# Optimization experiments

Hardware: AMD Instinct MI355X
Metric: run time of the kernel (lower is better)

## Reference

```python
import jax, jax.numpy as jnp
import numpy as np


def setup_inputs() -> dict:
    key = jax.random.key(0)
    ks = jax.random.split(key, 8)
    B, H, W, C = 4, 64, 64, 64
    Cf = C // 8
    x = jax.random.normal(ks[0], (B, H, W, C), dtype=jnp.float32)
    # 1x1 conv kernels stored as [C_in, C_out] (kernel_size=1)
    w_f = jax.random.normal(ks[1], (C, Cf), dtype=jnp.float32) * 0.05
    b_f = jax.random.normal(ks[2], (Cf,), dtype=jnp.float32) * 0.05
    w_g = jax.random.normal(ks[3], (C, Cf), dtype=jnp.float32) * 0.05
    b_g = jax.random.normal(ks[4], (Cf,), dtype=jnp.float32) * 0.05
    w_h = jax.random.normal(ks[5], (C, C), dtype=jnp.float32) * 0.05
    b_h = jax.random.normal(ks[6], (C,), dtype=jnp.float32) * 0.05
    gamma = jax.random.normal(ks[7], (1,), dtype=jnp.float32) * 0.1
    return {"x": x, "w_f": w_f, "b_f": b_f, "w_g": w_g, "b_g": b_g,
            "w_h": w_h, "b_h": b_h, "gamma": gamma}


def reference(x, w_f, b_f, w_g, b_g, w_h, b_h, gamma):
    B, H, W, C = x.shape
    N = H * W
    xf = x.reshape(B, N, C)  # 1x1 conv == per-pixel linear
    f = xf @ w_f + b_f       # [B, N, C/8]
    g = xf @ w_g + b_g       # [B, N, C/8]
    h = xf @ w_h + b_h       # [B, N, C]
    # attention_map[b, i, j] = <g_i, f_j>, softmax over last axis
    scores = jnp.einsum('bic,bjc->bij', g, f)  # [B, N, N]
    attn = jax.nn.softmax(scores, axis=-1)
    out = jnp.einsum('bij,bjc->bic', attn, h)  # [B, N, C]
    out = out.reshape(B, H, W, C)
    return gamma * out + x
```

## Files before the change

kernel.cpp:

```cpp
#include <hip/hip_runtime.h>
#include <hip/hip_bf16.h>

typedef __bf16 bf16;
typedef __bf16 bf16x8 __attribute__((ext_vector_type(8)));
typedef __bf16 bf16x4 __attribute__((ext_vector_type(4)));
typedef float floatx4 __attribute__((ext_vector_type(4)));

typedef int    aint    __attribute__((may_alias));
typedef long   along   __attribute__((may_alias));

#define NPIX 4096
#define BATCH 4
#define LOG2E 1.4426950408889634f
#define HT_BATCH 262144

__device__ inline bf16x8 zero8() {
    bf16x8 v;
    #pragma unroll
    for (int i = 0; i < 8; ++i) v[i] = (bf16)0.0f;
    return v;
}

__global__ __launch_bounds__(256) void proj_kernel(
    const float* __restrict__ x,
    const float* __restrict__ w_f, const float* __restrict__ b_f,
    const float* __restrict__ w_g, const float* __restrict__ b_g,
    const float* __restrict__ w_h, const float* __restrict__ b_h,
    bf16* __restrict__ fq, bf16* __restrict__ gq, unsigned char* __restrict__ hT)
{
    __shared__ bf16 xs[64 * 72];
    __shared__ bf16 wt[80 * 72];
    __shared__ float bs[80];
    const int tid = threadIdx.x;
    const int p0 = blockIdx.x * 64;

    {
        const float4* xg = (const float4*)(x + (long)p0 * 64);
        #pragma unroll
        for (int it = 0; it < 4; ++it) {
            int i4 = tid + it * 256;
            float4 v = xg[i4];
            int row = i4 >> 4, c4 = (i4 & 15) * 4;
            bf16x4 pk;
            pk[0] = (bf16)v.x; pk[1] = (bf16)v.y; pk[2] = (bf16)v.z; pk[3] = (bf16)v.w;
            *(bf16x4*)(&xs[row * 72 + c4]) = pk;
        }
    }
    for (int idx = tid; idx < 80 * 64; idx += 256) {
        int n = idx >> 6, c = idx & 63;
        float v = (n < 8) ? w_f[c * 8 + n]
                : (n < 16) ? w_g[c * 8 + (n - 8)]
                : w_h[c * 64 + (n - 16)];
        wt[n * 72 + c] = (bf16)v;
    }
    if (tid < 80)
        bs[tid] = (tid < 8) ? b_f[tid] : (tid < 16) ? b_g[tid - 8] : b_h[tid - 16];
    __syncthreads();

    const int wv = tid >> 6, lane = tid & 63;
    const int quad = lane >> 4, l15 = lane & 15;
    const int b = blockIdx.x >> 6;
    const int n0pix = (p0 & (NPIX - 1)) + wv * 16 + quad * 4;

    bf16x8 a0 = *(const bf16x8*)(&xs[(wv * 16 + l15) * 72 + quad * 8]);
    bf16x8 a1 = *(const bf16x8*)(&xs[(wv * 16 + l15) * 72 + 32 + quad * 8]);

    #pragma unroll
    for (int nt = 0; nt < 5; ++nt) {
        float bias = bs[nt * 16 + l15];
        floatx4 acc = {bias, bias, bias, bias};
        bf16x8 b0 = *(const bf16x8*)(&wt[(nt * 16 + l15) * 72 + quad * 8]);
        bf16x8 b1 = *(const bf16x8*)(&wt[(nt * 16 + l15) * 72 + 32 + quad * 8]);
        acc = __builtin_amdgcn_mfma_f32_16x16x32_bf16(a0, b0, acc, 0, 0, 0);
        acc = __builtin_amdgcn_mfma_f32_16x16x32_bf16(a1, b1, acc, 0, 0, 0);
        if (nt == 0) {
            #pragma unroll
            for (int r = 0; r < 4; ++r) {
                long P = (long)p0 + wv * 16 + quad * 4 + r;
                if (l15 < 8) fq[P * 8 + l15] = (bf16)acc[r];
                else         gq[P * 8 + (l15 - 8)] = (bf16)(acc[r] * LOG2E);
            }
        } else {
            int c = nt * 16 + l15 - 16;
            int pk = __builtin_amdgcn_cvt_pk_fp8_f32(acc[0], acc[1], 0, false);
            pk     = __builtin_amdgcn_cvt_pk_fp8_f32(acc[2], acc[3], pk, true);
            *(aint*)(hT + (long)b * HT_BATCH + (n0pix >> 5) * 2048
                     + c * 32 + (n0pix & 31)) = pk;
        }
    }
}

__global__ __launch_bounds__(256) void attn_kernel(
    const bf16* __restrict__ fq, const bf16* __restrict__ gq,
    const unsigned char* __restrict__ hT, float* __restrict__ partial)
{
    __shared__ char smem[4 * 2176];
    const int tid  = threadIdx.x;
    const int wv   = tid >> 6, lane = tid & 63;
    const int quad = lane >> 4, l15 = lane & 15;
    const int js   = blockIdx.x >> 8;
    const int ib   = blockIdx.x & 255;
    const int b    = ib >> 6, it = ib & 63;
    const long rowbase = (long)b * NPIX + it * 64 + wv * 16;
    const int jbase = js * 1024;

    bf16x8 gfrag = zero8();
    if (lane < 16) gfrag = *(const bf16x8*)(gq + (rowbase + lane) * 8);

    const bf16* Fb = fq + ((long)b * NPIX + jbase) * 8;
    const unsigned char* Hb = hT + (long)b * HT_BATCH + (jbase >> 5) * 2048
                            + (l15 * 32 + quad * 8);

    floatx4 acc[5];
    #pragma unroll
    for (int nt = 0; nt < 5; ++nt) acc[nt] = (floatx4){0.f, 0.f, 0.f, 0.f};
    const along ones = 0x3838383838383838L;
    char* Pw = smem + wv * 2176;

    for (int t = 0; t < 8; ++t) {
        along bfr[16];
        #pragma unroll
        for (int ks = 0; ks < 4; ++ks)
            #pragma unroll
            for (int nt = 0; nt < 4; ++nt)
                bfr[ks * 4 + nt] = *(const along*)(Hb + (t * 4 + ks) * 2048 + nt * 512);
        #pragma unroll
        for (int j8 = 0; j8 < 8; ++j8) {
            bf16x8 afrag = zero8();
            if (lane < 16) afrag = *(const bf16x8*)(Fb + (t * 128 + j8 * 16 + l15) * 8);
            floatx4 s = __builtin_amdgcn_mfma_f32_16x16x32_bf16(
                afrag, gfrag, (floatx4){0.f, 0.f, 0.f, 0.f}, 0, 0, 0);
            float e0 = __builtin_amdgcn_exp2f(s[0]);
            float e1 = __builtin_amdgcn_exp2f(s[1]);
            float e2 = __builtin_amdgcn_exp2f(s[2]);
            float e3 = __builtin_amdgcn_exp2f(s[3]);
            int pk = __builtin_amdgcn_cvt_pk_fp8_f32(e0, e1, 0, false);
            pk     = __builtin_amdgcn_cvt_pk_fp8_f32(e2, e3, pk, true);
            *(aint*)(Pw + l15 * 136 + j8 * 16 + quad * 4) = pk;
        }
        asm volatile("" ::: "memory");
        #pragma unroll
        for (int ks = 0; ks < 4; ++ks) {
            along pfrag = *(const along*)(Pw + l15 * 136 + ks * 32 + quad * 8);
            #pragma unroll
            for (int nt = 0; nt < 4; ++nt)
                acc[nt] = __builtin_amdgcn_mfma_f32_16x16x32_fp8_fp8(
                    pfrag, bfr[ks * 4 + nt], acc[nt], 0, 0, 0);
            acc[4] = __builtin_amdgcn_mfma_f32_16x16x32_fp8_fp8(pfrag, ones, acc[4], 0, 0, 0);
        }
    }

    float* pb = partial + ((long)js * (BATCH * NPIX) + rowbase) * 68;
    #pragma unroll
    for (int nt = 0; nt < 4; ++nt)
        #pragma unroll
        for (int r = 0; r < 4; ++r)
            pb[(quad * 4 + r) * 68 + nt * 16 + l15] = acc[nt][r];
    if (l15 == 0) {
        #pragma unroll
        for (int r = 0; r < 4; ++r)
            pb[(quad * 4 + r) * 68 + 64] = acc[4][r];
    }
}

__global__ __launch_bounds__(256) void reduce_kernel(
    const float* __restrict__ partial, const float* __restrict__ x,
    const float* __restrict__ gamma_p, float* __restrict__ out)
{
    const int tid = threadIdx.x;
    const long i  = (long)blockIdx.x * 32 + (tid >> 3);
    const int c0  = (tid & 7) * 8;
    const float* p = partial + i * 68;
    float4 n0 = {0.f, 0.f, 0.f, 0.f}, n1 = {0.f, 0.f, 0.f, 0.f};
    float den = 0.f;
    #pragma unroll
    for (int js = 0; js < 4; ++js) {
        const float* pj = p + (long)js * (BATCH * NPIX) * 68;
        float4 a = *(const float4*)(pj + c0);
        float4 c = *(const float4*)(pj + c0 + 4);
        n0.x += a.x; n0.y += a.y; n0.z += a.z; n0.w += a.w;
        n1.x += c.x; n1.y += c.y; n1.z += c.z; n1.w += c.w;
        den += pj[64];
    }
    const float rd = gamma_p[0] / den;
    const float* xr = x + i * 64 + c0;
    float* orow = out + i * 64 + c0;
    float4 xa = *(const float4*)xr, xb = *(const float4*)(xr + 4);
    float4 oa, ob;
    oa.x = n0.x * rd + xa.x; oa.y = n0.y * rd + xa.y;
    oa.z = n0.z * rd + xa.z; oa.w = n0.w * rd + xa.w;
    ob.x = n1.x * rd + xb.x; ob.y = n1.y * rd + xb.y;
    ob.z = n1.z * rd + xb.z; ob.w = n1.w * rd + xb.w;
    *(float4*)orow = oa; *(float4*)(orow + 4) = ob;
}

extern "C" void kernel_launch(void* const* d_in, const int* in_sizes, int n_in,
                              void* d_out, int out_size, void* d_ws, size_t ws_size,
                              hipStream_t stream) {
    const float* x     = (const float*)d_in[0];
    const float* w_f   = (const float*)d_in[1];
    const float* b_f   = (const float*)d_in[2];
    const float* w_g   = (const float*)d_in[3];
    const float* b_g   = (const float*)d_in[4];
    const float* w_h   = (const float*)d_in[5];
    const float* b_h   = (const float*)d_in[6];
    const float* gamma = (const float*)d_in[7];
    float* out = (float*)d_out;

    bf16* fq = (bf16*)d_ws;
    bf16* gq = fq + 16384 * 8;
    unsigned char* hT = (unsigned char*)(gq + 16384 * 8);
    float* partial = (float*)(hT + (long)BATCH * HT_BATCH);

    proj_kernel<<<256, 256, 0, stream>>>(x, w_f, b_f, w_g, b_g, w_h, b_h, fq, gq, hT);
    attn_kernel<<<1024, 256, 0, stream>>>(fq, gq, hT, partial);
    reduce_kernel<<<512, 256, 0, stream>>>(partial, x, gamma, out);
}
```

Measured before the change: 118.1 us.

## Double-buffer P tiles and H fragments to overlap score and PV phases

Splits the attention inner loop into load, score/exp and PV phases, and software-pipelines them with two LDS P buffers and two register sets of H fragments. The next tile's scores and H loads are issued before the current tile's PV MFMAs, which is meant to hide global-load and exp latency behind matrix work. It also adds a launch_bounds occupancy hint of 4 and doubles per-wave shared memory. The extra 16 longs of fragment registers raise register pressure and could cause spills or lower occupancy.

Measured after the change: 117.5 us. No clear change (-0.6%).

```diff
diff --git a/kernel.cpp b/kernel.cpp
--- a/kernel.cpp
+++ b/kernel.cpp
@@ -90,11 +90,50 @@
     }
 }
 
-__global__ __launch_bounds__(256) void attn_kernel(
+__device__ inline void load_bfr(along* bfr, const unsigned char* Hb, int t) {
+    #pragma unroll
+    for (int ks = 0; ks < 4; ++ks)
+        #pragma unroll
+        for (int nt = 0; nt < 4; ++nt)
+            bfr[ks * 4 + nt] = *(const along*)(Hb + (t * 4 + ks) * 2048 + nt * 512);
+}
+
+__device__ inline void s_phase(const bf16* __restrict__ Fb, int t, bf16x8 gfrag,
+                               char* Pbuf, int lane, int l15, int quad) {
+    #pragma unroll
+    for (int j8 = 0; j8 < 8; ++j8) {
+        bf16x8 afrag = zero8();
+        if (lane < 16) afrag = *(const bf16x8*)(Fb + (t * 128 + j8 * 16 + l15) * 8);
+        floatx4 s = __builtin_amdgcn_mfma_f32_16x16x32_bf16(
+            afrag, gfrag, (floatx4){0.f, 0.f, 0.f, 0.f}, 0, 0, 0);
+        float e0 = __builtin_amdgcn_exp2f(s[0]);
+        float e1 = __builtin_amdgcn_exp2f(s[1]);
+        float e2 = __builtin_amdgcn_exp2f(s[2]);
+        float e3 = __builtin_amdgcn_exp2f(s[3]);
+        int pk = __builtin_amdgcn_cvt_pk_fp8_f32(e0, e1, 0, false);
+        pk     = __builtin_amdgcn_cvt_pk_fp8_f32(e2, e3, pk, true);
+        *(aint*)(Pbuf + l15 * 136 + j8 * 16 + quad * 4) = pk;
+    }
+}
+
+__device__ inline void pv_phase(const char* Pbuf, const along* bfr, along ones,
+                                floatx4* acc, int l15, int quad) {
+    #pragma unroll
+    for (int ks = 0; ks < 4; ++ks) {
+        along pfrag = *(const along*)(Pbuf + l15 * 136 + ks * 32 + quad * 8);
+        #pragma unroll
+        for (int nt = 0; nt < 4; ++nt)
+            acc[nt] = __builtin_amdgcn_mfma_f32_16x16x32_fp8_fp8(
+                pfrag, bfr[ks * 4 + nt], acc[nt], 0, 0, 0);
+        acc[4] = __builtin_amdgcn_mfma_f32_16x16x32_fp8_fp8(pfrag, ones, acc[4], 0, 0, 0);
+    }
+}
+
+__global__ __launch_bounds__(256, 4) void attn_kernel(
     const bf16* __restrict__ fq, const bf16* __restrict__ gq,
     const unsigned char* __restrict__ hT, float* __restrict__ partial)
 {
-    __shared__ char smem[4 * 2176];
+    __shared__ char smem[4 * 2 * 2176];
     const int tid  = threadIdx.x;
     const int wv   = tid >> 6, lane = tid & 63;
     const int quad = lane >> 4, l15 = lane & 15;
@@ -115,39 +154,29 @@
     #pragma unroll
     for (int nt = 0; nt < 5; ++nt) acc[nt] = (floatx4){0.f, 0.f, 0.f, 0.f};
     const along ones = 0x3838383838383838L;
-    char* Pw = smem + wv * 2176;
-
-    for (int t = 0; t < 8; ++t) {
-        along bfr[16];
-        #pragma unroll
-        for (int ks = 0; ks < 4; ++ks)
-            #pragma unroll
-            for (int nt = 0; nt < 4; ++nt)
-                bfr[ks * 4 + nt] = *(const along*)(Hb + (t * 4 + ks) * 2048 + nt * 512);
-        #pragma unroll
-        for (int j8 = 0; j8 < 8; ++j8) {
-            bf16x8 afrag = zero8();
-            if (lane < 16) afrag = *(const bf16x8*)(Fb + (t * 128 + j8 * 16 + l15) * 8);
-            floatx4 s = __builtin_amdgcn_mfma_f32_16x16x32_bf16(
-                afrag, gfrag, (floatx4){0.f, 0.f, 0.f, 0.f}, 0, 0, 0);
-            float e0 = __builtin_amdgcn_exp2f(s[0]);
-            float e1 = __builtin_amdgcn_exp2f(s[1]);
-            float e2 = __builtin_amdgcn_exp2f(s[2]);
-            float e3 = __builtin_amdgcn_exp2f(s[3]);
-            int pk = __builtin_amdgcn_cvt_pk_fp8_f32(e0, e1, 0, false);
-            pk     = __builtin_amdgcn_cvt_pk_fp8_f32(e2, e3, pk, true);
-            *(aint*)(Pw + l15 * 136 + j8 * 16 + quad * 4) = pk;
+    char* P0 = smem + wv * 4352;
+    char* P1 = P0 + 2176;
+
+    along bfrA[16], bfrB[16];
+
+    load_bfr(bfrA, Hb, 0);
+    s_phase(Fb, 0, gfrag, P0, lane, l15, quad);
+
+    #pragma unroll
+    for (int tt = 0; tt < 4; ++tt) {
+        const int t = 2 * tt;
+        if (t + 1 < 8) {
+            load_bfr(bfrB, Hb, t + 1);
+            s_phase(Fb, t + 1, gfrag, P1, lane, l15, quad);
         }
         asm volatile("" ::: "memory");
-        #pragma unroll
-        for (int ks = 0; ks < 4; ++ks) {
-            along pfrag = *(const along*)(Pw + l15 * 136 + ks * 32 + quad * 8);
-            #pragma unroll
-            for (int nt = 0; nt < 4; ++nt)
-                acc[nt] = __builtin_amdgcn_mfma_f32_16x16x32_fp8_fp8(
-                    pfrag, bfr[ks * 4 + nt], acc[nt], 0, 0, 0);
-            acc[4] = __builtin_amdgcn_mfma_f32_16x16x32_fp8_fp8(pfrag, ones, acc[4], 0, 0, 0);
-        }
+        pv_phase(P0, bfrA, ones, acc, l15, quad);
+        if (t + 2 < 8) {
+            load_bfr(bfrA, Hb, t + 2);
+            s_phase(Fb, t + 2, gfrag, P0, lane, l15, quad);
+        }
+        asm volatile("" ::: "memory");
+        pv_phase(P1, bfrB, ones, acc, l15, quad);
     }
 
     float* pb = partial + ((long)js * (BATCH * NPIX) + rowbase) * 68;
```

## Fuse split-KV reduction into attention kernel via in-block LDS reduction

Applied to the files above, without the earlier changes.

The attention kernel now uses 512-thread blocks. Each block covers 32 query rows, and its 8 waves split those rows into 2 groups across 4 key-range quarters. The partial numerators and denominators are reduced in shared memory, then normalized and combined with the residual in the same kernel. This removes the global partial buffer, its write and re-read traffic, and the separate reduce-kernel launch. In exchange it uses more LDS per block, adds block-level syncs, and halves the block count. The projection kernel's weight staging loads are also rewritten to read coalesced.

Result: faster. 105.5 us (-10.7%).

```diff
diff --git a/kernel.cpp b/kernel.cpp
--- a/kernel.cpp
+++ b/kernel.cpp
@@ -46,12 +46,16 @@
             *(bf16x4*)(&xs[row * 72 + c4]) = pk;
         }
     }
-    for (int idx = tid; idx < 80 * 64; idx += 256) {
-        int n = idx >> 6, c = idx & 63;
-        float v = (n < 8) ? w_f[c * 8 + n]
-                : (n < 16) ? w_g[c * 8 + (n - 8)]
-                : w_h[c * 64 + (n - 16)];
-        wt[n * 72 + c] = (bf16)v;
+    for (int idx = tid; idx < 512; idx += 256) {
+        int c = idx >> 3, n = idx & 7;
+        wt[n * 72 + c]       = (bf16)w_f[idx];
+        wt[(8 + n) * 72 + c] = (bf16)w_g[idx];
+    }
+    #pragma unroll
+    for (int it = 0; it < 16; ++it) {
+        int idx = tid + it * 256;
+        int c = idx >> 6, n = idx & 63;
+        wt[(16 + n) * 72 + c] = (bf16)w_h[idx];
     }
     if (tid < 80)
         bs[tid] = (tid < 8) ? b_f[tid] : (tid < 16) ? b_g[tid - 8] : b_h[tid - 16];
@@ -90,19 +94,23 @@
     }
 }
 
-__global__ __launch_bounds__(256) void attn_kernel(
+#define PBYTES 2176
+#define REDOFF (8 * PBYTES)
+#define LDSTOT (REDOFF + 128 * 68 * 4)
+
+__global__ __launch_bounds__(512, 4) void attn_kernel(
     const bf16* __restrict__ fq, const bf16* __restrict__ gq,
-    const unsigned char* __restrict__ hT, float* __restrict__ partial)
+    const unsigned char* __restrict__ hT, const float* __restrict__ x,
+    const float* __restrict__ gamma_p, float* __restrict__ out)
 {
-    __shared__ char smem[4 * 2176];
+    __shared__ char smem[LDSTOT];
     const int tid  = threadIdx.x;
     const int wv   = tid >> 6, lane = tid & 63;
     const int quad = lane >> 4, l15 = lane & 15;
-    const int js   = blockIdx.x >> 8;
-    const int ib   = blockIdx.x & 255;
-    const int b    = ib >> 6, it = ib & 63;
-    const long rowbase = (long)b * NPIX + it * 64 + wv * 16;
-    const int jbase = js * 1024;
+    const int igrp = wv & 1, jq = wv >> 1;
+    const int b    = blockIdx.x >> 7, it = blockIdx.x & 127;
+    const long rowbase = (long)b * NPIX + it * 32 + igrp * 16;
+    const int jbase = jq * 1024;
 
     bf16x8 gfrag = zero8();
     if (lane < 16) gfrag = *(const bf16x8*)(gq + (rowbase + lane) * 8);
@@ -115,7 +123,7 @@
     #pragma unroll
     for (int nt = 0; nt < 5; ++nt) acc[nt] = (floatx4){0.f, 0.f, 0.f, 0.f};
     const along ones = 0x3838383838383838L;
-    char* Pw = smem + wv * 2176;
+    char* Pw = smem + wv * PBYTES;
 
     for (int t = 0; t < 8; ++t) {
         along bfr[16];
@@ -148,50 +156,45 @@
                     pfrag, bfr[ks * 4 + nt], acc[nt], 0, 0, 0);
             acc[4] = __builtin_amdgcn_mfma_f32_16x16x32_fp8_fp8(pfrag, ones, acc[4], 0, 0, 0);
         }
-    }
-
-    float* pb = partial + ((long)js * (BATCH * NPIX) + rowbase) * 68;
-    #pragma unroll
-    for (int nt = 0; nt < 4; ++nt)
-        #pragma unroll
-        for (int r = 0; r < 4; ++r)
-            pb[(quad * 4 + r) * 68 + nt * 16 + l15] = acc[nt][r];
-    if (l15 == 0) {
-        #pragma unroll
-        for (int r = 0; r < 4; ++r)
-            pb[(quad * 4 + r) * 68 + 64] = acc[4][r];
-    }
-}
-
-__global__ __launch_bounds__(256) void reduce_kernel(
-    const float* __restrict__ partial, const float* __restrict__ x,
-    const float* __restrict__ gamma_p, float* __restrict__ out)
-{
-    const int tid = threadIdx.x;
-    const long i  = (long)blockIdx.x * 32 + (tid >> 3);
-    const int c0  = (tid & 7) * 8;
-    const float* p = partial + i * 68;
-    float4 n0 = {0.f, 0.f, 0.f, 0.f}, n1 = {0.f, 0.f, 0.f, 0.f};
-    float den = 0.f;
-    #pragma unroll
-    for (int js = 0; js < 4; ++js) {
-        const float* pj = p + (long)js * (BATCH * NPIX) * 68;
-        float4 a = *(const float4*)(pj + c0);
-        float4 c = *(const float4*)(pj + c0 + 4);
-        n0.x += a.x; n0.y += a.y; n0.z += a.z; n0.w += a.w;
-        n1.x += c.x; n1.y += c.y; n1.z += c.z; n1.w += c.w;
-        den += pj[64];
-    }
-    const float rd = gamma_p[0] / den;
-    const float* xr = x + i * 64 + c0;
-    float* orow = out + i * 64 + c0;
-    float4 xa = *(const float4*)xr, xb = *(const float4*)(xr + 4);
-    float4 oa, ob;
-    oa.x = n0.x * rd + xa.x; oa.y = n0.y * rd + xa.y;
-    oa.z = n0.z * rd + xa.z; oa.w = n0.w * rd + xa.w;
-    ob.x = n1.x * rd + xb.x; ob.y = n1.y * rd + xb.y;
-    ob.z = n1.z * rd + xb.z; ob.w = n1.w * rd + xb.w;
-    *(float4*)orow = oa; *(float4*)(orow + 4) = ob;
+        asm volatile("" ::: "memory");
+    }
+    __syncthreads();
+
+    float* red = (float*)(smem + REDOFF);
+    {
+        const int rb = (jq * 32 + igrp * 16 + quad * 4) * 68;
+        #pragma unroll
+        for (int nt = 0; nt < 4; ++nt)
+            #pragma unroll
+            for (int r = 0; r < 4; ++r)
+                red[rb + r * 68 + nt * 16 + l15] = acc[nt][r];
+        if (l15 == 0) {
+            #pragma unroll
+            for (int r = 0; r < 4; ++r)
+                red[rb + r * 68 + 64] = acc[4][r];
+        }
+    }
+    __syncthreads();
+
+    {
+        const int row = tid >> 4, c0 = (tid & 15) * 4;
+        float4 n = {0.f, 0.f, 0.f, 0.f};
+        float den = 0.f;
+        #pragma unroll
+        for (int q = 0; q < 4; ++q) {
+            const float* rr = red + (q * 32 + row) * 68;
+            float4 v = *(const float4*)(rr + c0);
+            n.x += v.x; n.y += v.y; n.z += v.z; n.w += v.w;
+            den += rr[64];
+        }
+        const float rd = gamma_p[0] / den;
+        const long off = ((long)b * NPIX + it * 32 + row) * 64 + c0;
+        float4 xv = *(const float4*)(x + off);
+        float4 o;
+        o.x = n.x * rd + xv.x; o.y = n.y * rd + xv.y;
+        o.z = n.z * rd + xv.z; o.w = n.w * rd + xv.w;
+        *(float4*)(out + off) = o;
+    }
 }
 
 extern "C" void kernel_launch(void* const* d_in, const int* in_sizes, int n_in,
@@ -210,9 +213,7 @@
     bf16* fq = (bf16*)d_ws;
     bf16* gq = fq + 16384 * 8;
     unsigned char* hT = (unsigned char*)(gq + 16384 * 8);
-    float* partial = (float*)(hT + (long)BATCH * HT_BATCH);
 
     proj_kernel<<<256, 256, 0, stream>>>(x, w_f, b_f, w_g, b_g, w_h, b_h, fq, gq, hT);
-    attn_kernel<<<1024, 256, 0, stream>>>(fq, gq, hT, partial);
-    reduce_kernel<<<512, 256, 0, stream>>>(partial, x, gamma, out);
-}
+    attn_kernel<<<512, 512, 0, stream>>>(fq, gq, hT, x, gamma, out);
+}
```

## Stage F/H tiles in shared memory with double buffering and shuffle P via bpermute

Applied to the files above, without the earlier changes.

The attention kernel now uses 512-thread blocks covering 128 query rows, so eight waves share cooperatively loaded, double-buffered LDS tiles of F and fp8 H instead of each wave loading its own copies from global memory. The P-matrix shuffle that went through an LDS round trip is replaced by ds_bpermute register exchanges. The projection kernel's weight loads are reorganized for coalesced reads. This cuts redundant global traffic per wave, at the cost of a __syncthreads per tile and a different grid split.

Measured after the change: 110.4 us. 6.6% less time.

```diff
diff --git a/kernel.cpp b/kernel.cpp
--- a/kernel.cpp
+++ b/kernel.cpp
@@ -8,6 +8,7 @@
 
 typedef int    aint    __attribute__((may_alias));
 typedef long   along   __attribute__((may_alias));
+typedef float4 afloat4 __attribute__((may_alias));
 
 #define NPIX 4096
 #define BATCH 4
@@ -46,12 +47,16 @@
             *(bf16x4*)(&xs[row * 72 + c4]) = pk;
         }
     }
-    for (int idx = tid; idx < 80 * 64; idx += 256) {
-        int n = idx >> 6, c = idx & 63;
-        float v = (n < 8) ? w_f[c * 8 + n]
-                : (n < 16) ? w_g[c * 8 + (n - 8)]
-                : w_h[c * 64 + (n - 16)];
-        wt[n * 72 + c] = (bf16)v;
+    for (int idx = tid; idx < 512; idx += 256) {
+        int c = idx >> 3, n = idx & 7;
+        wt[n * 72 + c]       = (bf16)w_f[idx];
+        wt[(8 + n) * 72 + c] = (bf16)w_g[idx];
+    }
+    #pragma unroll
+    for (int it = 0; it < 16; ++it) {
+        int idx = tid + it * 256;
+        int c = idx >> 6, n = idx & 63;
+        wt[(16 + n) * 72 + c] = (bf16)w_h[idx];
     }
     if (tid < 80)
         bs[tid] = (tid < 8) ? b_f[tid] : (tid < 16) ? b_g[tid - 8] : b_h[tid - 16];
@@ -90,67 +95,88 @@
     }
 }
 
-__global__ __launch_bounds__(256) void attn_kernel(
+__global__ __launch_bounds__(512, 4) void attn_kernel(
     const bf16* __restrict__ fq, const bf16* __restrict__ gq,
     const unsigned char* __restrict__ hT, float* __restrict__ partial)
 {
-    __shared__ char smem[4 * 2176];
+    __shared__ char Ft[2][2048];
+    __shared__ char Ht[2][8192];
     const int tid  = threadIdx.x;
     const int wv   = tid >> 6, lane = tid & 63;
     const int quad = lane >> 4, l15 = lane & 15;
-    const int js   = blockIdx.x >> 8;
-    const int ib   = blockIdx.x & 255;
-    const int b    = ib >> 6, it = ib & 63;
-    const long rowbase = (long)b * NPIX + it * 64 + wv * 16;
-    const int jbase = js * 1024;
+    const int jh   = blockIdx.x >> 7;
+    const int b    = (blockIdx.x >> 5) & 3;
+    const int it   = blockIdx.x & 31;
+    const long rowbase = (long)b * NPIX + it * 128 + wv * 16;
+    const int jbase = jh * 1024;
 
     bf16x8 gfrag = zero8();
     if (lane < 16) gfrag = *(const bf16x8*)(gq + (rowbase + lane) * 8);
 
-    const bf16* Fb = fq + ((long)b * NPIX + jbase) * 8;
-    const unsigned char* Hb = hT + (long)b * HT_BATCH + (jbase >> 5) * 2048
-                            + (l15 * 32 + quad * 8);
+    const char* Fg = (const char*)(fq + ((long)b * NPIX + jbase) * 8);
+    const char* Hg = (const char*)hT + (long)b * HT_BATCH + (jbase >> 5) * 2048;
 
     floatx4 acc[5];
     #pragma unroll
     for (int nt = 0; nt < 5; ++nt) acc[nt] = (floatx4){0.f, 0.f, 0.f, 0.f};
     const along ones = 0x3838383838383838L;
-    char* Pw = smem + wv * 2176;
+
+    const int idx_lo = (((quad & 1) * 2) * 16 + l15) * 4;
+    const int idx_hi = idx_lo + 64;
+    const bool sel_b = (quad >> 1) != 0;
+
+    *(afloat4*)(Ht[0] + tid * 16) = *(const float4*)(Hg + tid * 16);
+    if (tid < 128)
+        *(afloat4*)(Ft[0] + tid * 16) = *(const float4*)(Fg + tid * 16);
+    __syncthreads();
 
     for (int t = 0; t < 8; ++t) {
-        along bfr[16];
-        #pragma unroll
-        for (int ks = 0; ks < 4; ++ks)
-            #pragma unroll
-            for (int nt = 0; nt < 4; ++nt)
-                bfr[ks * 4 + nt] = *(const along*)(Hb + (t * 4 + ks) * 2048 + nt * 512);
+        const int buf = t & 1;
+        if (t < 7) {
+            *(afloat4*)(Ht[buf ^ 1] + tid * 16) =
+                *(const float4*)(Hg + (t + 1) * 8192 + tid * 16);
+            if (tid < 128)
+                *(afloat4*)(Ft[buf ^ 1] + tid * 16) =
+                    *(const float4*)(Fg + (t + 1) * 2048 + tid * 16);
+        }
+        int pk[8];
         #pragma unroll
         for (int j8 = 0; j8 < 8; ++j8) {
             bf16x8 afrag = zero8();
-            if (lane < 16) afrag = *(const bf16x8*)(Fb + (t * 128 + j8 * 16 + l15) * 8);
+            if (lane < 16)
+                afrag = *(const bf16x8*)(Ft[buf] + (j8 * 16 + l15) * 16);
             floatx4 s = __builtin_amdgcn_mfma_f32_16x16x32_bf16(
                 afrag, gfrag, (floatx4){0.f, 0.f, 0.f, 0.f}, 0, 0, 0);
             float e0 = __builtin_amdgcn_exp2f(s[0]);
             float e1 = __builtin_amdgcn_exp2f(s[1]);
             float e2 = __builtin_amdgcn_exp2f(s[2]);
             float e3 = __builtin_amdgcn_exp2f(s[3]);
-            int pk = __builtin_amdgcn_cvt_pk_fp8_f32(e0, e1, 0, false);
-            pk     = __builtin_amdgcn_cvt_pk_fp8_f32(e2, e3, pk, true);
-            *(aint*)(Pw + l15 * 136 + j8 * 16 + quad * 4) = pk;
-        }
-        asm volatile("" ::: "memory");
+            int p = __builtin_amdgcn_cvt_pk_fp8_f32(e0, e1, 0, false);
+            pk[j8] = __builtin_amdgcn_cvt_pk_fp8_f32(e2, e3, p, true);
+        }
         #pragma unroll
         for (int ks = 0; ks < 4; ++ks) {
-            along pfrag = *(const along*)(Pw + l15 * 136 + ks * 32 + quad * 8);
+            int pa = pk[2 * ks], pb = pk[2 * ks + 1];
+            int lo0 = __builtin_amdgcn_ds_bpermute(idx_lo, pa);
+            int lo1 = __builtin_amdgcn_ds_bpermute(idx_lo, pb);
+            int hi0 = __builtin_amdgcn_ds_bpermute(idx_hi, pa);
+            int hi1 = __builtin_amdgcn_ds_bpermute(idx_hi, pb);
+            unsigned lo = (unsigned)(sel_b ? lo1 : lo0);
+            unsigned hi = (unsigned)(sel_b ? hi1 : hi0);
+            along pfrag = (along)(((unsigned long)hi << 32) | lo);
             #pragma unroll
-            for (int nt = 0; nt < 4; ++nt)
+            for (int nt = 0; nt < 4; ++nt) {
+                along bfrag = *(const along*)(Ht[buf] + ks * 2048 + nt * 512
+                                              + l15 * 32 + quad * 8);
                 acc[nt] = __builtin_amdgcn_mfma_f32_16x16x32_fp8_fp8(
-                    pfrag, bfr[ks * 4 + nt], acc[nt], 0, 0, 0);
+                    pfrag, bfrag, acc[nt], 0, 0, 0);
+            }
             acc[4] = __builtin_amdgcn_mfma_f32_16x16x32_fp8_fp8(pfrag, ones, acc[4], 0, 0, 0);
         }
-    }
-
-    float* pb = partial + ((long)js * (BATCH * NPIX) + rowbase) * 68;
+        __syncthreads();
+    }
+
+    float* pb = partial + ((long)jh * (BATCH * NPIX) + rowbase) * 68;
     #pragma unroll
     for (int nt = 0; nt < 4; ++nt)
         #pragma unroll
@@ -213,6 +239,6 @@
     float* partial = (float*)(hT + (long)BATCH * HT_BATCH);
 
     proj_kernel<<<256, 256, 0, stream>>>(x, w_f, b_f, w_g, b_g, w_h, b_h, fq, gq, hT);
-    attn_kernel<<<1024, 256, 0, stream>>>(fq, gq, hT, partial);
+    attn_kernel<<<512, 512, 0, stream>>>(fq, gq, hT, partial);
     reduce_kernel<<<512, 256, 0, stream>>>(partial, x, gamma, out);
 }
```
